# Performance work log

Hardware: AMD Instinct MI355X
Metric: run time of the kernel (lower is better)

Reference implementation:

```python
import jax, jax.numpy as jnp
import numpy as np
import math

NUM_HEADS = 8
FDIM = 64
NUM_BUCKETS = 32
MAX_DISTANCE = 128


def _relative_position_bucket(rel_pos, num_buckets=NUM_BUCKETS, max_distance=MAX_DISTANCE):
    nb = num_buckets // 2
    ret = (rel_pos >= 0).astype(jnp.int32) * nb
    n = jnp.abs(rel_pos)
    max_exact = nb // 2
    is_small = n < max_exact
    # safe log: clamp n to >=1 where large-branch is unused
    val_large = max_exact + (
        jnp.log(jnp.maximum(n, 1).astype(jnp.float32) / max_exact)
        / math.log(max_distance / max_exact) * (nb - max_exact)
    ).astype(jnp.int32)
    val_large = jnp.minimum(val_large, nb - 1)
    return ret + jnp.where(is_small, n, val_large)


def setup_inputs() -> dict:
    key = jax.random.key(0)
    k = jax.random.split(key, 5)
    B, Nin, F, T = 4, 64, FDIM, 1024
    N = NUM_HEADS * FDIM
    x = jax.random.normal(k[0], (B, Nin, F, T), dtype=jnp.float32)
    # kaiming_normal: std = 1/sqrt(fan_in)
    w_in = jax.random.normal(k[1], (NUM_HEADS, Nin), dtype=jnp.float32) / np.sqrt(Nin)
    w_qk = jax.random.normal(k[2], (2 * N, N), dtype=jnp.float32) / np.sqrt(N)
    w_out = jax.random.normal(k[3], (Nin, NUM_HEADS), dtype=jnp.float32) / np.sqrt(NUM_HEADS)
    rel_bias = jax.random.normal(k[4], (NUM_BUCKETS, NUM_HEADS), dtype=jnp.float32) * 0.02
    return {"x": x, "w_in": w_in, "w_qk": w_qk, "w_out": w_out, "rel_bias": rel_bias}


def reference(x, w_in, w_qk, w_out, rel_bias):
    B, Nin, F, T = x.shape
    h, f = NUM_HEADS, FDIM
    scale = f ** (-0.5)
    # proj_in: 1x1 conv2d Nin -> h
    xi = jnp.einsum('bcft,hc->bhft', x, w_in)          # [B,h,F,T]
    xr = xi.reshape(B, h * f, T)                        # b (h f) t
    v = xr.reshape(B, h, f, T).transpose(0, 1, 3, 2)    # [B,h,T,f]
    # qk: 1x1 conv1d N -> 2N
    qk = jnp.einsum('bct,dc->bdt', xr, w_qk)            # [B,2N,T]
    qk = qk.reshape(B, h, 2 * f, T).transpose(0, 1, 3, 2)  # [B,h,T,2f]
    q, k = qk[..., :f], qk[..., f:]
    sim = jnp.einsum('bhnd,bhmd->bhnm', q, k)           # [B,h,T,T]
    # relative position bias
    q_pos = jnp.arange(T)
    k_pos = jnp.arange(T)
    rel = k_pos[None, :] - q_pos[:, None]               # [T,T]
    buckets = _relative_position_bucket(rel)
    bias = rel_bias[buckets]                            # [T,T,h]
    bias = bias.transpose(2, 0, 1)[None]                # [1,h,T,T]
    sim = (sim + bias) * scale
    attn = jax.nn.softmax(sim, axis=-1)
    out = jnp.einsum('bhnm,bhmd->bhnd', attn, v)        # [B,h,T,f]
    out = out.transpose(0, 1, 3, 2)                     # [B,h,f,T]
    out = jnp.einsum('bhft,ch->bcft', out, w_out)       # [B,Nin,F,T]
    return out
```

## Files before the change

kernel.cpp:

```cpp
#include <hip/hip_runtime.h>
#include <math.h>

#define QSCALE 0.18033688011112042f

typedef __attribute__((ext_vector_type(4))) float  f32x4;
typedef __attribute__((ext_vector_type(2))) float  f32x2;
typedef __attribute__((ext_vector_type(8))) short  bf16x8;
typedef __attribute__((ext_vector_type(4))) short  bf16x4;
typedef __attribute__((ext_vector_type(4))) int    i32x4;

static __device__ __forceinline__ short f2bf(float f) {
    union { float f; unsigned u; } v; v.f = f;
    unsigned r = v.u + 0x7fffu + ((v.u >> 16) & 1u);
    return (short)(r >> 16);
}
static __device__ __forceinline__ int pk2bf(float a, float b) {
    return ((int)f2bf(a) & 0xffff) | ((int)f2bf(b) << 16);
}

#define MFMA16(A,B,C) __builtin_amdgcn_mfma_f32_16x16x32_bf16(A, B, C, 0, 0, 0)

__global__ void k_prep(const float* __restrict__ wqk, short* __restrict__ wqk_b) {
    int i = blockIdx.x * 256 + threadIdx.x;
    int D = i >> 9;
    float s = (D & 64) ? 1.0f : QSCALE;
    wqk_b[i] = f2bf(wqk[i] * s);
}

__global__ __launch_bounds__(256) void k_proj_in(
    const float* __restrict__ x, const float* __restrict__ w_in,
    short* __restrict__ xi_v, short* __restrict__ xr_t)
{
    __shared__ float w_s[512];
    __shared__ __align__(16) short tr[64 * 72];
    int tid = threadIdx.x;
    int tx = tid & 31, fy = tid >> 5;
    int tb = blockIdx.x, fb = blockIdx.y, b = blockIdx.z;
    w_s[tid] = w_in[tid & 511];
    w_s[(tid + 256) & 511] = w_in[(tid + 256) & 511];
    __syncthreads();

    int f = fb * 8 + fy;
    int t = tb * 64 + tx * 2;
    float acc[8][2];
    #pragma unroll
    for (int h = 0; h < 8; h++) { acc[h][0] = 0.f; acc[h][1] = 0.f; }

    const float* xp = x + ((size_t)b * 64 * 64 + (size_t)f) * 1024 + t;
    f32x2 buf[8];
    #pragma unroll
    for (int i = 0; i < 8; i++) buf[i] = *(const f32x2*)&xp[(size_t)i * 65536];
    #pragma unroll
    for (int c8 = 0; c8 < 64; c8 += 8) {
        f32x2 cur[8];
        #pragma unroll
        for (int i = 0; i < 8; i++) cur[i] = buf[i];
        if (c8 + 8 < 64) {
            #pragma unroll
            for (int i = 0; i < 8; i++)
                buf[i] = *(const f32x2*)&xp[(size_t)(c8 + 8 + i) * 65536];
        }
        #pragma unroll
        for (int i = 0; i < 8; i++)
            #pragma unroll
            for (int h = 0; h < 8; h++) {
                float wv = w_s[h * 64 + c8 + i];
                acc[h][0] = fmaf(cur[i][0], wv, acc[h][0]);
                acc[h][1] = fmaf(cur[i][1], wv, acc[h][1]);
            }
    }
    #pragma unroll
    for (int h = 0; h < 8; h++)
        *(int*)&xi_v[(((size_t)b * 8 + h) * 64 + f) * 1024 + t] = pk2bf(acc[h][0], acc[h][1]);
    #pragma unroll
    for (int h = 0; h < 8; h++) {
        tr[(tx * 2 + 0) * 72 + h * 8 + fy] = f2bf(acc[h][0]);
        tr[(tx * 2 + 1) * 72 + h * 8 + fy] = f2bf(acc[h][1]);
    }
    __syncthreads();
    int h2 = tid & 7, trow = tid >> 3;
    #pragma unroll
    for (int i = 0; i < 2; i++) {
        int t2 = trow + i * 32;
        i32x4 v = *(const i32x4*)&tr[t2 * 72 + h2 * 8];
        *(i32x4*)&xr_t[((size_t)b * 1024 + tb * 64 + t2) * 512 + h2 * 64 + fb * 8] = v;
    }
}

__global__ __launch_bounds__(256, 4) void k_qk(
    const short* __restrict__ wqk_b, const short* __restrict__ xr_t,
    short* __restrict__ qk_t)
{
    __shared__ __align__(16) short As[64 * 72];
    __shared__ __align__(16) short Bs[64 * 72];
    int tid = threadIdx.x;
    int w = tid >> 6, lane = tid & 63;
    int quad = lane >> 4, l16 = lane & 15;
    int t0 = blockIdx.x * 64;
    int Dt = blockIdx.y;
    int b  = blockIdx.z;

    f32x4 acc[4];
    #pragma unroll
    for (int tt = 0; tt < 4; tt++) acc[tt] = (f32x4){0.f,0.f,0.f,0.f};

    const short* Ag = wqk_b + (size_t)Dt * 64 * 512;
    const short* Bg = xr_t + ((size_t)b * 1024 + t0) * 512;

    int s_row = tid >> 2, s_col = (tid & 3) * 16;

    for (int kk = 0; kk < 512; kk += 64) {
        __syncthreads();
        #pragma unroll
        for (int i = 0; i < 2; i++) {
            *(i32x4*)&As[s_row * 72 + s_col + i * 8] =
                *(const i32x4*)&Ag[(size_t)s_row * 512 + kk + s_col + i * 8];
            *(i32x4*)&Bs[s_row * 72 + s_col + i * 8] =
                *(const i32x4*)&Bg[(size_t)s_row * 512 + kk + s_col + i * 8];
        }
        __syncthreads();
        bf16x8 af[2];
        #pragma unroll
        for (int kc = 0; kc < 2; kc++)
            af[kc] = *(const bf16x8*)&As[(w * 16 + l16) * 72 + kc * 32 + quad * 8];
        #pragma unroll
        for (int tt = 0; tt < 4; tt++) {
            bf16x8 bf0 = *(const bf16x8*)&Bs[(tt * 16 + l16) * 72 + quad * 8];
            bf16x8 bf1 = *(const bf16x8*)&Bs[(tt * 16 + l16) * 72 + 32 + quad * 8];
            acc[tt] = MFMA16(af[0], bf0, acc[tt]);
            acc[tt] = MFMA16(af[1], bf1, acc[tt]);
        }
    }
    int h = Dt >> 1;
    int d2 = (Dt & 1) * 64 + w * 16 + quad * 4;
    #pragma unroll
    for (int tt = 0; tt < 4; tt++) {
        bf16x4 pk;
        pk.x = f2bf(acc[tt][0]); pk.y = f2bf(acc[tt][1]);
        pk.z = f2bf(acc[tt][2]); pk.w = f2bf(acc[tt][3]);
        int t = t0 + tt * 16 + l16;
        *(bf16x4*)&qk_t[(((size_t)b * 8 + h) * 1024 + t) * 128 + d2] = pk;
    }
}

__global__ __launch_bounds__(256, 4) void k_attn(
    const short* __restrict__ qk_t, const short* __restrict__ xi_v,
    const float* __restrict__ rel_bias, float* __restrict__ o_part,
    float* __restrict__ lsum)
{
    __shared__ __align__(16) short Ks[64 * 72];
    __shared__ __align__(16) short Vs[64 * 72];
    __shared__ __align__(16) short Ps[4][16 * 72];
    __shared__ float elut[2048];
    int tid = threadIdx.x;
    int w = tid >> 6, lane = tid & 63;
    int quad = lane >> 4, l16 = lane & 15;
    int nb = blockIdx.x, bh = blockIdx.y, mh = blockIdx.z;
    int h = bh & 7;
    int n_base = nb * 64;

    for (int i = tid; i < 2047; i += 256) {
        int rel = i - 1023;
        int ret = (rel >= 0) ? 16 : 0;
        int na = rel < 0 ? -rel : rel;
        int idx;
        if (na < 8) idx = ret + na;
        else {
            int vl = 8 + (int)(log2f((float)na * 0.125f) * 2.0f);
            vl = vl > 15 ? 15 : vl;
            idx = ret + vl;
        }
        elut[i] = exp2f(rel_bias[idx * 8 + h] * QSCALE);
    }

    const short* qb = qk_t + (size_t)bh * (1024 * 128);
    const short* vb = xi_v + (size_t)bh * (64 * 1024);

    bf16x8 qf[2];
    #pragma unroll
    for (int kk = 0; kk < 2; kk++)
        qf[kk] = *(const bf16x8*)&qb[(size_t)(n_base + w * 16 + l16) * 128 + kk * 32 + quad * 8];

    f32x4 acc_o[4];
    #pragma unroll
    for (int dt = 0; dt < 4; dt++) acc_o[dt] = (f32x4){0.f,0.f,0.f,0.f};
    float l_st = 0.f;

    int srow = tid >> 2;
    int soff = (tid & 3) * 16;
    int m0 = mh * 512;
    i32x4 gk[2], gv[2];
    #pragma unroll
    for (int i = 0; i < 2; i++) {
        gk[i] = *(const i32x4*)&qb[(size_t)(m0 + srow) * 128 + 64 + soff + i * 8];
        gv[i] = *(const i32x4*)&vb[(size_t)srow * 1024 + m0 + soff + i * 8];
    }

    __syncthreads();

    #pragma unroll 1
    for (int it = 0; it < 8; it++) {
        *(i32x4*)&Ks[srow * 72 + soff]     = gk[0];
        *(i32x4*)&Ks[srow * 72 + soff + 8] = gk[1];
        *(i32x4*)&Vs[srow * 72 + soff]     = gv[0];
        *(i32x4*)&Vs[srow * 72 + soff + 8] = gv[1];
        __syncthreads();
        if (it < 7) {
            int m1 = m0 + 64;
            #pragma unroll
            for (int i = 0; i < 2; i++) {
                gk[i] = *(const i32x4*)&qb[(size_t)(m1 + srow) * 128 + 64 + soff + i * 8];
                gv[i] = *(const i32x4*)&vb[(size_t)srow * 1024 + m1 + soff + i * 8];
            }
        }

        f32x4 s[4];
        #pragma unroll
        for (int mt = 0; mt < 4; mt++) {
            bf16x8 kf0 = *(const bf16x8*)&Ks[(mt * 16 + l16) * 72 + quad * 8];
            bf16x8 kf1 = *(const bf16x8*)&Ks[(mt * 16 + l16) * 72 + 32 + quad * 8];
            f32x4 tacc = (f32x4){0.f,0.f,0.f,0.f};
            tacc = MFMA16(kf0, qf[0], tacc);
            tacc = MFMA16(kf1, qf[1], tacc);
            s[mt] = tacc;
        }

        int n = n_base + w * 16 + l16;
        #pragma unroll
        for (int mt = 0; mt < 4; mt++) {
            int rel0 = m0 + mt * 16 + quad * 4 - n + 1023;
            #pragma unroll
            for (int j = 0; j < 4; j++) {
                float p = exp2f(s[mt][j]) * elut[rel0 + j];
                s[mt][j] = p;
                l_st += p;
            }
        }
        #pragma unroll
        for (int mt = 0; mt < 4; mt++) {
            bf16x4 pk;
            pk.x = f2bf(s[mt][0]); pk.y = f2bf(s[mt][1]);
            pk.z = f2bf(s[mt][2]); pk.w = f2bf(s[mt][3]);
            *(bf16x4*)&Ps[w][l16 * 72 + mt * 16 + quad * 4] = pk;
        }
        #pragma unroll
        for (int si = 0; si < 2; si++) {
            bf16x8 pf = *(const bf16x8*)&Ps[w][l16 * 72 + si * 32 + quad * 8];
            #pragma unroll
            for (int dt = 0; dt < 4; dt++) {
                bf16x8 vf = *(const bf16x8*)&Vs[(dt * 16 + l16) * 72 + si * 32 + quad * 8];
                acc_o[dt] = MFMA16(pf, vf, acc_o[dt]);
            }
        }
        m0 += 64;
        __syncthreads();
    }
    #pragma unroll
    for (int dt = 0; dt < 4; dt++)
        *(f32x4*)&o_part[(((size_t)mh * 32 + bh) * 64 + dt * 16 + l16) * 1024 + n_base + w * 16 + quad * 4] = acc_o[dt];
    l_st += __shfl_xor(l_st, 16);
    l_st += __shfl_xor(l_st, 32);
    if (quad == 0)
        lsum[((size_t)bh * 2 + mh) * 1024 + n_base + w * 16 + l16] = l_st;
}

__global__ __launch_bounds__(512) void k_proj_out(
    const float* __restrict__ o_part, const float* __restrict__ lsum,
    const float* __restrict__ w_out, float* __restrict__ out)
{
    __shared__ float w_s[512];
    __shared__ float o_s[8][64];
    int tid = threadIdx.x;
    int tx = tid & 63, ty = tid >> 6;
    int tb = blockIdx.x, f = blockIdx.y, b = blockIdx.z;
    w_s[tid] = w_out[tid];
    int t = tb * 64 + tx;
    int bh = b * 8 + ty;
    float l0 = lsum[((size_t)bh * 2 + 0) * 1024 + t];
    float l1 = lsum[((size_t)bh * 2 + 1) * 1024 + t];
    float o0 = o_part[((size_t)(0 * 32 + bh) * 64 + f) * 1024 + t];
    float o1 = o_part[((size_t)(1 * 32 + bh) * 64 + f) * 1024 + t];
    o_s[ty][tx] = (o0 + o1) / (l0 + l1);
    __syncthreads();
    float ov[8];
    #pragma unroll
    for (int hh = 0; hh < 8; hh++) ov[hh] = o_s[hh][tx];
    #pragma unroll
    for (int j = 0; j < 8; j++) {
        int c = ty * 8 + j;
        float a = 0.f;
        #pragma unroll
        for (int hh = 0; hh < 8; hh++) a = fmaf(ov[hh], w_s[c * 8 + hh], a);
        out[(((size_t)b * 64 + c) * 64 + f) * 1024 + t] = a;
    }
}

extern "C" void kernel_launch(void* const* d_in, const int* in_sizes, int n_in,
                              void* d_out, int out_size, void* d_ws, size_t ws_size,
                              hipStream_t stream)
{
    const float* x        = (const float*)d_in[0];
    const float* w_in     = (const float*)d_in[1];
    const float* w_qk     = (const float*)d_in[2];
    const float* w_out    = (const float*)d_in[3];
    const float* rel_bias = (const float*)d_in[4];
    float* out = (float*)d_out;

    char* ws = (char*)d_ws;
    short* wqk_b  = (short*)(ws);
    short* xi_v   = (short*)(ws + (size_t)1  * (1 << 20));
    short* xr_t   = (short*)(ws + (size_t)5  * (1 << 20));
    short* qk_t   = (short*)(ws + (size_t)9  * (1 << 20));
    float* o_part = (float*)(ws + (size_t)17 * (1 << 20));
    float* lsum   = (float*)(ws + (size_t)33 * (1 << 20));

    hipLaunchKernelGGL(k_prep,     dim3(2048),       dim3(256), 0, stream, w_qk, wqk_b);
    hipLaunchKernelGGL(k_proj_in,  dim3(16, 8, 4),   dim3(256), 0, stream, x, w_in, xi_v, xr_t);
    hipLaunchKernelGGL(k_qk,       dim3(16, 16, 4),  dim3(256), 0, stream, wqk_b, xr_t, qk_t);
    hipLaunchKernelGGL(k_attn,     dim3(16, 32, 2),  dim3(256), 0, stream, qk_t, xi_v, rel_bias, o_part, lsum);
    hipLaunchKernelGGL(k_proj_out, dim3(16, 64, 4),  dim3(512), 0, stream, o_part, lsum, w_out, out);
}
```

Baseline: 162.2 us.

## Fuse weight prep into proj_in, prefetch qk tiles, remap blocks for XCD locality

```diff
diff --git a/kernel.cpp b/kernel.cpp
--- a/kernel.cpp
+++ b/kernel.cpp
@@ -20,15 +20,9 @@
 
 #define MFMA16(A,B,C) __builtin_amdgcn_mfma_f32_16x16x32_bf16(A, B, C, 0, 0, 0)
 
-__global__ void k_prep(const float* __restrict__ wqk, short* __restrict__ wqk_b) {
-    int i = blockIdx.x * 256 + threadIdx.x;
-    int D = i >> 9;
-    float s = (D & 64) ? 1.0f : QSCALE;
-    wqk_b[i] = f2bf(wqk[i] * s);
-}
-
 __global__ __launch_bounds__(256) void k_proj_in(
     const float* __restrict__ x, const float* __restrict__ w_in,
+    const float* __restrict__ wqk, short* __restrict__ wqk_b,
     short* __restrict__ xi_v, short* __restrict__ xr_t)
 {
     __shared__ float w_s[512];
@@ -36,6 +30,17 @@
     int tid = threadIdx.x;
     int tx = tid & 31, fy = tid >> 5;
     int tb = blockIdx.x, fb = blockIdx.y, b = blockIdx.z;
+
+    {
+        int gi = (((b * 8 + fb) * 16 + tb) * 256 + tid) * 4;
+        f32x4 wv = *(const f32x4*)&wqk[gi];
+        float s = ((gi >> 9) & 64) ? 1.0f : QSCALE;
+        bf16x4 pk;
+        pk.x = f2bf(wv[0] * s); pk.y = f2bf(wv[1] * s);
+        pk.z = f2bf(wv[2] * s); pk.w = f2bf(wv[3] * s);
+        *(bf16x4*)&wqk_b[gi] = pk;
+    }
+
     w_s[tid] = w_in[tid & 511];
     w_s[(tid + 256) & 511] = w_in[(tid + 256) & 511];
     __syncthreads();
@@ -96,33 +101,46 @@
     int tid = threadIdx.x;
     int w = tid >> 6, lane = tid & 63;
     int quad = lane >> 4, l16 = lane & 15;
-    int t0 = blockIdx.x * 64;
-    int Dt = blockIdx.y;
-    int b  = blockIdx.z;
+    int bid = blockIdx.x;
+    int wg = (bid & 7) * 128 + (bid >> 3);
+    int Dt = wg & 15;
+    int tb = (wg >> 4) & 15;
+    int b  = wg >> 8;
+    int t0 = tb * 64;
 
     f32x4 acc[4];
     #pragma unroll
     for (int tt = 0; tt < 4; tt++) acc[tt] = (f32x4){0.f,0.f,0.f,0.f};
 
-    const short* Ag = wqk_b + (size_t)Dt * 64 * 512;
-    const short* Bg = xr_t + ((size_t)b * 1024 + t0) * 512;
-
     int s_row = tid >> 2, s_col = (tid & 3) * 16;
+    const short* Ag = wqk_b + ((size_t)Dt * 64 + s_row) * 512;
+    const short* Bg = xr_t + ((size_t)b * 1024 + t0 + s_row) * 512;
+
+    i32x4 ga[2], gb[2];
+    #pragma unroll
+    for (int i = 0; i < 2; i++) {
+        ga[i] = *(const i32x4*)&Ag[s_col + i * 8];
+        gb[i] = *(const i32x4*)&Bg[s_col + i * 8];
+    }
 
     for (int kk = 0; kk < 512; kk += 64) {
+        *(i32x4*)&As[s_row * 72 + s_col]     = ga[0];
+        *(i32x4*)&As[s_row * 72 + s_col + 8] = ga[1];
+        *(i32x4*)&Bs[s_row * 72 + s_col]     = gb[0];
+        *(i32x4*)&Bs[s_row * 72 + s_col + 8] = gb[1];
         __syncthreads();
-        #pragma unroll
-        for (int i = 0; i < 2; i++) {
-            *(i32x4*)&As[s_row * 72 + s_col + i * 8] =
-                *(const i32x4*)&Ag[(size_t)s_row * 512 + kk + s_col + i * 8];
-            *(i32x4*)&Bs[s_row * 72 + s_col + i * 8] =
-                *(const i32x4*)&Bg[(size_t)s_row * 512 + kk + s_col + i * 8];
-        }
-        __syncthreads();
+        if (kk < 448) {
+            #pragma unroll
+            for (int i = 0; i < 2; i++) {
+                ga[i] = *(const i32x4*)&Ag[kk + 64 + s_col + i * 8];
+                gb[i] = *(const i32x4*)&Bg[kk + 64 + s_col + i * 8];
+            }
+        }
         bf16x8 af[2];
         #pragma unroll
         for (int kc = 0; kc < 2; kc++)
             af[kc] = *(const bf16x8*)&As[(w * 16 + l16) * 72 + kc * 32 + quad * 8];
+        __builtin_amdgcn_s_setprio(1);
         #pragma unroll
         for (int tt = 0; tt < 4; tt++) {
             bf16x8 bf0 = *(const bf16x8*)&Bs[(tt * 16 + l16) * 72 + quad * 8];
@@ -130,6 +148,8 @@
             acc[tt] = MFMA16(af[0], bf0, acc[tt]);
             acc[tt] = MFMA16(af[1], bf1, acc[tt]);
         }
+        __builtin_amdgcn_s_setprio(0);
+        __syncthreads();
     }
     int h = Dt >> 1;
     int d2 = (Dt & 1) * 64 + w * 16 + quad * 4;
@@ -155,7 +175,11 @@
     int tid = threadIdx.x;
     int w = tid >> 6, lane = tid & 63;
     int quad = lane >> 4, l16 = lane & 15;
-    int nb = blockIdx.x, bh = blockIdx.y, mh = blockIdx.z;
+    int bid = blockIdx.x;
+    int wg = (bid & 7) * 128 + (bid >> 3);
+    int nb = wg & 15;
+    int mh = (wg >> 4) & 1;
+    int bh = wg >> 5;
     int h = bh & 7;
     int n_base = nb * 64;
 
@@ -215,6 +239,7 @@
         }
 
         f32x4 s[4];
+        __builtin_amdgcn_s_setprio(1);
         #pragma unroll
         for (int mt = 0; mt < 4; mt++) {
             bf16x8 kf0 = *(const bf16x8*)&Ks[(mt * 16 + l16) * 72 + quad * 8];
@@ -224,6 +249,7 @@
             tacc = MFMA16(kf1, qf[1], tacc);
             s[mt] = tacc;
         }
+        __builtin_amdgcn_s_setprio(0);
 
         int n = n_base + w * 16 + l16;
         #pragma unroll
@@ -243,6 +269,7 @@
             pk.z = f2bf(s[mt][2]); pk.w = f2bf(s[mt][3]);
             *(bf16x4*)&Ps[w][l16 * 72 + mt * 16 + quad * 4] = pk;
         }
+        __builtin_amdgcn_s_setprio(1);
         #pragma unroll
         for (int si = 0; si < 2; si++) {
             bf16x8 pf = *(const bf16x8*)&Ps[w][l16 * 72 + si * 32 + quad * 8];
@@ -252,6 +279,7 @@
                 acc_o[dt] = MFMA16(pf, vf, acc_o[dt]);
             }
         }
+        __builtin_amdgcn_s_setprio(0);
         m0 += 64;
         __syncthreads();
     }
@@ -314,9 +342,8 @@
     float* o_part = (float*)(ws + (size_t)17 * (1 << 20));
     float* lsum   = (float*)(ws + (size_t)33 * (1 << 20));
 
-    hipLaunchKernelGGL(k_prep,     dim3(2048),       dim3(256), 0, stream, w_qk, wqk_b);
-    hipLaunchKernelGGL(k_proj_in,  dim3(16, 8, 4),   dim3(256), 0, stream, x, w_in, xi_v, xr_t);
-    hipLaunchKernelGGL(k_qk,       dim3(16, 16, 4),  dim3(256), 0, stream, wqk_b, xr_t, qk_t);
-    hipLaunchKernelGGL(k_attn,     dim3(16, 32, 2),  dim3(256), 0, stream, qk_t, xi_v, rel_bias, o_part, lsum);
+    hipLaunchKernelGGL(k_proj_in,  dim3(16, 8, 4),   dim3(256), 0, stream, x, w_in, w_qk, wqk_b, xi_v, xr_t);
+    hipLaunchKernelGGL(k_qk,       dim3(1024),       dim3(256), 0, stream, wqk_b, xr_t, qk_t);
+    hipLaunchKernelGGL(k_attn,     dim3(1024),       dim3(256), 0, stream, qk_t, xi_v, rel_bias, o_part, lsum);
     hipLaunchKernelGGL(k_proj_out, dim3(16, 64, 4),  dim3(512), 0, stream, o_part, lsum, w_out, out);
 }
```

New measurement: 160.8 us. About the same (-0.9%).
